# Optimization experiments

Measured on AMD Instinct MI355X. Metric: run time of the kernel, lower is better.

The kernel has to match this reference:

```python
import jax, jax.numpy as jnp
import numpy as np

B, H, N, D = 2, 16, 4096, 64
NUM_PROJS = 8
BLOCK_SIZE = 256
SAMPLE_SIZE = 256
SCALE = D ** -0.5  # default scale = dim ** -0.5


def _unit_hamming_distance_array(size_n):
    # Gray-code permutation so that adjacent hash buckets differ in one bit
    a = np.array([0, 1], dtype=np.int32)
    for _ in range(size_n - 1):
        a = np.concatenate([a, np.flip(a) + a.shape[0]])
    return a

_PERM = jnp.asarray(_unit_hamming_distance_array(NUM_PROJS))
_ENC = jnp.asarray(2 ** np.arange(NUM_PROJS, dtype=np.int32))  # [num_projs]


def lsh_hash(x, proj_dir):
    # x: [b,h,n,d], proj_dir: [d,r] -> bucket id per token: [b,h,n]
    proj = jnp.einsum('bhnd,dr->bhnr', x, proj_dir)
    bin_ids = jnp.sum((proj > 0).astype(jnp.int32) * _ENC, axis=-1)
    return _PERM[bin_ids]


def attn_lse(q, k, v, scale):
    # exact softmax attention returning output and log-sum-exp
    s = jnp.einsum('...md,...nd->...mn', q, k) * scale
    lse = jax.nn.logsumexp(s, axis=-1, keepdims=True)
    out = jnp.einsum('...mn,...nv->...mv', jnp.exp(s - lse), v)
    return out, lse


def gather_seq(x, idx):
    # gather along the sequence axis (axis=2); broadcasts over last dim
    return jnp.take_along_axis(x, idx[..., None], axis=2)


def add_self_attentions(attn1, lse1, attn2, lse2):
    # combine two un-normalized softmax attentions via their lse's
    c = jax.nn.sigmoid(lse1 - lse2)  # = 1/(1+exp(lse2-lse1))
    attn = c * attn1 + (1.0 - c) * attn2
    lse = jnp.logaddexp(lse1, lse2)
    return attn, lse


def setup_inputs() -> dict:
    key = jax.random.key(0)
    kq, kk, kv, kp, ks = jax.random.split(key, 5)
    return {
        'query': jax.random.normal(kq, (B, H, N, D), jnp.float32),
        'key': jax.random.normal(kk, (B, H, N, D), jnp.float32),
        'value': jax.random.normal(kv, (B, H, N, D), jnp.float32),
        'proj_dir': jax.random.normal(kp, (D, NUM_PROJS), jnp.float32),
        'sampled_set': jax.random.randint(ks, (B, H, SAMPLE_SIZE), 0, N, dtype=jnp.int32),
    }


def reference(query, key, value, proj_dir, sampled_set):
    # --- LSH bucketing + stable sort of queries/keys by bucket id ---
    q_idx = jnp.argsort(lsh_hash(query, proj_dir), axis=2, stable=True)
    k_idx = jnp.argsort(lsh_hash(key, proj_dir), axis=2, stable=True)
    q_idx_inv = jnp.argsort(q_idx, axis=2, stable=True)

    q_s = gather_seq(query, q_idx)
    k_s = gather_seq(key, k_idx)
    v_s = gather_seq(value, k_idx)

    # --- block-diagonal attention in sorted order ---
    nb = N // BLOCK_SIZE
    q_b = q_s.reshape(B, H, nb, BLOCK_SIZE, D)
    k_b = k_s.reshape(B, H, nb, BLOCK_SIZE, D)
    v_b = v_s.reshape(B, H, nb, BLOCK_SIZE, D)
    attn_blk, lse_blk = attn_lse(q_b, k_b, v_b, SCALE)
    attn_blk = attn_blk.reshape(B, H, N, D)
    lse_blk = lse_blk.reshape(B, H, N, 1)
    # un-sort back to original query order
    attn_blk = gather_seq(attn_blk, q_idx_inv)
    lse_blk = gather_seq(lse_blk, q_idx_inv)

    # --- uniformly sampled residual attention, importance-weighted ---
    k_sub = gather_seq(key, sampled_set)
    v_sub = gather_seq(value, sampled_set)
    attn_res, lse_res = attn_lse(query, k_sub, v_sub, SCALE)
    lse_res = lse_res + jnp.log(N / SAMPLE_SIZE)

    attn, lse = add_self_attentions(attn_blk, lse_blk, attn_res, lse_res)
    return attn
```

## Files before the change

### kernel.cpp

```cpp
#include <hip/hip_runtime.h>
#include <hip/hip_bf16.h>
#include <math.h>

#define BH_ 32
#define N_ 4096
#define D_ 64
#define SAMP_ 256
#define SCALE_ 0.125f
#define LOG16_ 2.7725887222397811f
#define HPAD 68

typedef __attribute__((ext_vector_type(4))) float f32x4;
typedef __attribute__((ext_vector_type(8))) short bf16x8;
typedef __attribute__((ext_vector_type(4))) short bf16x4;

static __device__ __forceinline__ unsigned pack2(float a, float b) {
    union { __hip_bfloat162 h; unsigned u; } c;
    c.h = __float22bfloat162_rn(make_float2(a, b));
    return c.u;
}

static __device__ __forceinline__ bf16x8 cvt8v(f32x4 a, f32x4 b) {
    union { unsigned u[4]; bf16x8 v; } r;
    r.u[0] = pack2(a[0], a[1]); r.u[1] = pack2(a[2], a[3]);
    r.u[2] = pack2(b[0], b[1]); r.u[3] = pack2(b[2], b[3]);
    return r.v;
}

static __device__ __forceinline__ bf16x8 cvt8(const float* p) {
    return cvt8v(*(const f32x4*)p, *(const f32x4*)(p + 4));
}

__global__ __launch_bounds__(128) void hash_kernel(
    const float* __restrict__ q, const float* __restrict__ k,
    const float* __restrict__ pd,
    unsigned char* __restrict__ qbuck, unsigned char* __restrict__ kbuck)
{
    extern __shared__ char smraw[];
    float*  Xs  = (float*)smraw;
    double* Pdl = (double*)(smraw + 128 * HPAD * 4);

    int tid = threadIdx.x;
    const float* src = blockIdx.y ? k : q;
    unsigned char* dst = blockIdx.y ? kbuck : qbuck;
    size_t tok0 = (size_t)blockIdx.x * 128;

    {
        int d = tid >> 1, r0 = (tid & 1) * 4;
#pragma unroll
        for (int j = 0; j < 4; ++j)
            Pdl[d * 8 + r0 + j] = (double)pd[d * 8 + r0 + j];
    }
    {
        const float4* src4 = (const float4*)(src + tok0 * D_);
        for (int i = tid; i < 128 * 16; i += 128) {
            int r = i >> 4, c = i & 15;
            *(float4*)&Xs[r * HPAD + c * 4] = src4[i];
        }
    }
    __syncthreads();

    float xr[64];
#pragma unroll
    for (int c = 0; c < 16; ++c)
        *(float4*)&xr[c * 4] = *(const float4*)&Xs[tid * HPAD + c * 4];

    double acc[8];
#pragma unroll
    for (int r = 0; r < 8; ++r) acc[r] = 0.0;
#pragma unroll
    for (int d = 0; d < 64; ++d) {
        double x = (double)xr[d];
        const double* pr = Pdl + d * 8;
#pragma unroll
        for (int r = 0; r < 8; ++r) acc[r] += x * pr[r];
    }
    int bin = 0;
#pragma unroll
    for (int r = 0; r < 8; ++r)
        if (acc[r] > 0.0) bin |= (1 << r);
    dst[tok0 + tid] = (unsigned char)(bin ^ (bin >> 1));
}

__global__ __launch_bounds__(256) void sort_kernel(
    const unsigned char* __restrict__ qbuck,
    const unsigned char* __restrict__ kbuck,
    int* __restrict__ q_idx, int* __restrict__ k_idx)
{
    __shared__ unsigned short hist[64][256];
    __shared__ unsigned int   binstart[256];
    __shared__ alignas(16) unsigned char bl[N_];

    int bh = blockIdx.x, tensor = blockIdx.y;
    const unsigned char* buck = (tensor ? kbuck : qbuck) + bh * N_;
    int* idx_out = (tensor ? k_idx : q_idx) + bh * N_;
    int t = threadIdx.x;

    ((uint4*)bl)[t] = ((const uint4*)buck)[t];
    {
        uint4* h4 = (uint4*)&hist[0][0];
        for (int i = t; i < 2048; i += 256) h4[i] = make_uint4(0, 0, 0, 0);
    }
    __syncthreads();

    if (t < 64) {
        for (int u = 0; u < 64; ++u) hist[t][bl[t * 64 + u]]++;
    }
    __syncthreads();

    {
        unsigned run = 0;
        for (int tt = 0; tt < 64; ++tt) {
            unsigned c = hist[tt][t];
            hist[tt][t] = (unsigned short)run;
            run += c;
        }
        binstart[t] = run;
    }
    __syncthreads();

    if (t < 64) {
        unsigned b0 = binstart[t*4], b1 = binstart[t*4+1],
                 b2 = binstart[t*4+2], b3 = binstart[t*4+3];
        unsigned s = b0 + b1 + b2 + b3, p = s;
#pragma unroll
        for (int d = 1; d < 64; d <<= 1) {
            unsigned y = __shfl_up(p, d);
            if (t >= d) p += y;
        }
        unsigned e = p - s;
        binstart[t*4]   = e;
        binstart[t*4+1] = e + b0;
        binstart[t*4+2] = e + b0 + b1;
        binstart[t*4+3] = e + b0 + b1 + b2;
    }
    __syncthreads();

    if (t < 64) {
        for (int u = 0; u < 64; ++u) {
            int tok = t * 64 + u;
            int b = bl[tok];
            int pos = (int)(binstart[b] + hist[t][b]);
            hist[t][b]++;
            idx_out[pos] = tok;
        }
    }
}

static __device__ __forceinline__ void compute_chunk16(
    const short* __restrict__ Ks, unsigned vtr, float bias,
    const bf16x8 (&qf)[2], int ll, int lg,
    f32x4 (&o)[4], float& lsum)
{
#pragma unroll
    for (int ks2 = 0; ks2 < 4; ++ks2) {
        unsigned pbu[4];
#pragma unroll
        for (int t = 0; t < 2; ++t) {
            int kt = ks2 * 2 + t;
            f32x4 s = {0.f, 0.f, 0.f, 0.f};
#pragma unroll
            for (int ks = 0; ks < 2; ++ks) {
                bf16x8 a = *(const bf16x8*)&Ks[kt * 1024 + ks * 512 + lg * 128 + ll * 8];
                s = __builtin_amdgcn_mfma_f32_16x16x32_bf16(a, qf[ks], s, 0, 0, 0);
            }
            f32x4 e;
#pragma unroll
            for (int r = 0; r < 4; ++r) e[r] = __expf(fmaf(s[r], SCALE_, bias));
            lsum += (e[0] + e[1]) + (e[2] + e[3]);
            pbu[t*2]   = pack2(e[0], e[1]);
            pbu[t*2+1] = pack2(e[2], e[3]);
        }
        bf16x8 pb;
        { union { unsigned u[4]; bf16x8 v; } c;
          c.u[0]=pbu[0]; c.u[1]=pbu[1]; c.u[2]=pbu[2]; c.u[3]=pbu[3]; pb = c.v; }

        bf16x4 tr[4][2];
#pragma unroll
        for (int dt = 0; dt < 4; ++dt) {
            asm volatile("ds_read_b64_tr_b16 %0, %1 offset:%2"
                         : "=v"(tr[dt][0]) : "v"(vtr), "i"(ks2 * 4096 + dt * 128));
            asm volatile("ds_read_b64_tr_b16 %0, %1 offset:%2"
                         : "=v"(tr[dt][1]) : "v"(vtr), "i"(ks2 * 4096 + dt * 128 + 2048));
        }
        asm volatile("s_waitcnt lgkmcnt(0)" ::: "memory");
        __builtin_amdgcn_sched_barrier(0);
#pragma unroll
        for (int dt = 0; dt < 4; ++dt) {
            union { bf16x4 h[2]; bf16x8 v; } va;
            va.h[0] = tr[dt][0]; va.h[1] = tr[dt][1];
            o[dt] = __builtin_amdgcn_mfma_f32_16x16x32_bf16(va.v, pb, o[dt], 0, 0, 0);
        }
    }
}

__global__ __launch_bounds__(1024, 8) void fused_attn(
    const float* __restrict__ query, const float* __restrict__ key,
    const float* __restrict__ value, const int* __restrict__ q_idx,
    const int* __restrict__ k_idx, const int* __restrict__ sampled,
    float* __restrict__ out)
{
    __shared__ short Ksm[8192];
    __shared__ short Vsm[8192];
    int wg = blockIdx.x, bh = wg >> 4, blk = wg & 15;
    int tid = threadIdx.x, w = tid >> 6, l = tid & 63, lg = l >> 4, ll = l & 15;
    size_t base = (size_t)bh * N_;

    int s_krow = ((tid >> 7) << 4) | (tid & 15);
    int s_kd   = ((tid >> 6) & 1) * 32 + ((tid >> 4) & 3) * 8;
    int s_vrow = ((tid >> 5) << 2) | ((tid >> 1) & 3);
    int s_vd   = ((tid >> 3) & 3) * 16 + (tid & 1) * 8;

    const int* kidxA = k_idx + base + blk * 256;
    const int* kidxB = sampled + bh * SAMP_;
    int kI0 = kidxA[s_krow], kI1 = kidxA[128 + s_krow];
    int kI2 = kidxB[s_krow], kI3 = kidxB[128 + s_krow];
    int vI0 = kidxA[s_vrow], vI1 = kidxA[128 + s_vrow];
    int vI2 = kidxB[s_vrow], vI3 = kidxB[128 + s_vrow];

    const int* qidx = q_idx + base + blk * 256 + w * 16;
    int qr = qidx[ll];
    const float* qp = query + (base + (size_t)qr) * D_ + lg * 8;
    bf16x8 qf[2] = { cvt8(qp), cvt8(qp + 32) };

    f32x4 o[4];
#pragma unroll
    for (int dt = 0; dt < 4; ++dt) { f32x4 z = {0.f,0.f,0.f,0.f}; o[dt] = z; }
    float lsum = 0.f;
    unsigned vtr = (unsigned)(unsigned long long)(void*)&Vsm[0] + lg * 512 + ll * 8;

#define STAGE_(KI, VI) do { \
        const float* kp_ = key   + (base + (size_t)(KI)) * D_ + s_kd; \
        const float* vp_ = value + (base + (size_t)(VI)) * D_ + s_vd; \
        bf16x8 kv_ = cvt8(kp_), vv_ = cvt8(vp_); \
        *(bf16x8*)&Ksm[tid * 8] = kv_; \
        *(bf16x8*)&Vsm[tid * 8] = vv_; } while (0)

    STAGE_(kI0, vI0); __syncthreads();
    compute_chunk16(Ksm, vtr, 0.f, qf, ll, lg, o, lsum);
    __syncthreads(); STAGE_(kI1, vI1); __syncthreads();
    compute_chunk16(Ksm, vtr, 0.f, qf, ll, lg, o, lsum);
    __syncthreads(); STAGE_(kI2, vI2); __syncthreads();
    compute_chunk16(Ksm, vtr, LOG16_, qf, ll, lg, o, lsum);
    __syncthreads(); STAGE_(kI3, vI3); __syncthreads();
    compute_chunk16(Ksm, vtr, LOG16_, qf, ll, lg, o, lsum);
#undef STAGE_

    lsum += __shfl_xor(lsum, 16);
    lsum += __shfl_xor(lsum, 32);

    float dn = 1.f / lsum;
    float* orow = out + (base + (size_t)qr) * D_ + lg * 4;
#pragma unroll
    for (int dt = 0; dt < 4; ++dt) {
        f32x4 v = o[dt] * dn;
        *(f32x4*)&orow[dt * 16] = v;
    }
}

extern "C" void kernel_launch(void* const* d_in, const int* in_sizes, int n_in,
                              void* d_out, int out_size, void* d_ws, size_t ws_size,
                              hipStream_t stream)
{
    const float* query = (const float*)d_in[0];
    const float* key   = (const float*)d_in[1];
    const float* value = (const float*)d_in[2];
    const float* pd    = (const float*)d_in[3];
    const int*   samp  = (const int*)d_in[4];
    float* out = (float*)d_out;

    char* ws = (char*)d_ws;
    unsigned char* qbuck = (unsigned char*)ws;
    unsigned char* kbuck = qbuck + (size_t)BH_ * N_;
    int* q_idx = (int*)(ws + 262144);
    int* k_idx = (int*)(ws + 262144 + 524288);

    size_t hash_lds = 128 * HPAD * 4 + 512 * 8;
    hipLaunchKernelGGL(hash_kernel, dim3(BH_ * N_ / 128, 2), dim3(128),
                       hash_lds, stream, query, key, pd, qbuck, kbuck);
    hipLaunchKernelGGL(sort_kernel, dim3(BH_, 2), dim3(256), 0, stream,
                       qbuck, kbuck, q_idx, k_idx);
    hipLaunchKernelGGL(fused_attn, dim3(512), dim3(1024), 0, stream,
                       query, key, value, q_idx, k_idx, samp, out);
}
```

Before: 90.32 us.

## Restructure attention into per-wave register-prefetched K/V chunks without block barriers

Instead of the workgroup cooperatively staging 128-key chunks into shared memory with __syncthreads, each wave now loads its own 32-key chunks. K fragments go straight into registers and V goes into a private LDS slice read back with transpose reads. The next chunk's global loads and the index loads two chunks ahead are issued before the current compute, so memory latency overlaps with MFMA work. The workgroup shrinks to 512 threads over 128 queries, doubling the grid. In exchange, each wave reads K/V for its own 16-query group, multiplying global/L2 traffic per block, and register pressure rises.

Result: slower. 328.7 us (+263.9%).

```diff
diff --git a/kernel.cpp b/kernel.cpp
--- a/kernel.cpp
+++ b/kernel.cpp
@@ -63,7 +63,7 @@
     float xr[64];
 #pragma unroll
     for (int c = 0; c < 16; ++c)
-        *(float4*)&xr[c * 4] = *(const float4*)&Xs[tid * HPAD + c * 4];
+        *(f32x4*)&xr[c * 4] = *(const f32x4*)&Xs[tid * HPAD + c * 4];
 
     double acc[8];
 #pragma unroll
@@ -147,78 +147,27 @@
     }
 }
 
-static __device__ __forceinline__ void compute_chunk16(
-    const short* __restrict__ Ks, unsigned vtr, float bias,
-    const bf16x8 (&qf)[2], int ll, int lg,
-    f32x4 (&o)[4], float& lsum)
-{
-#pragma unroll
-    for (int ks2 = 0; ks2 < 4; ++ks2) {
-        unsigned pbu[4];
-#pragma unroll
-        for (int t = 0; t < 2; ++t) {
-            int kt = ks2 * 2 + t;
-            f32x4 s = {0.f, 0.f, 0.f, 0.f};
-#pragma unroll
-            for (int ks = 0; ks < 2; ++ks) {
-                bf16x8 a = *(const bf16x8*)&Ks[kt * 1024 + ks * 512 + lg * 128 + ll * 8];
-                s = __builtin_amdgcn_mfma_f32_16x16x32_bf16(a, qf[ks], s, 0, 0, 0);
-            }
-            f32x4 e;
-#pragma unroll
-            for (int r = 0; r < 4; ++r) e[r] = __expf(fmaf(s[r], SCALE_, bias));
-            lsum += (e[0] + e[1]) + (e[2] + e[3]);
-            pbu[t*2]   = pack2(e[0], e[1]);
-            pbu[t*2+1] = pack2(e[2], e[3]);
-        }
-        bf16x8 pb;
-        { union { unsigned u[4]; bf16x8 v; } c;
-          c.u[0]=pbu[0]; c.u[1]=pbu[1]; c.u[2]=pbu[2]; c.u[3]=pbu[3]; pb = c.v; }
-
-        bf16x4 tr[4][2];
-#pragma unroll
-        for (int dt = 0; dt < 4; ++dt) {
-            asm volatile("ds_read_b64_tr_b16 %0, %1 offset:%2"
-                         : "=v"(tr[dt][0]) : "v"(vtr), "i"(ks2 * 4096 + dt * 128));
-            asm volatile("ds_read_b64_tr_b16 %0, %1 offset:%2"
-                         : "=v"(tr[dt][1]) : "v"(vtr), "i"(ks2 * 4096 + dt * 128 + 2048));
-        }
-        asm volatile("s_waitcnt lgkmcnt(0)" ::: "memory");
-        __builtin_amdgcn_sched_barrier(0);
-#pragma unroll
-        for (int dt = 0; dt < 4; ++dt) {
-            union { bf16x4 h[2]; bf16x8 v; } va;
-            va.h[0] = tr[dt][0]; va.h[1] = tr[dt][1];
-            o[dt] = __builtin_amdgcn_mfma_f32_16x16x32_bf16(va.v, pb, o[dt], 0, 0, 0);
-        }
-    }
-}
-
-__global__ __launch_bounds__(1024, 8) void fused_attn(
+__global__ __launch_bounds__(512, 4) void fused_attn(
     const float* __restrict__ query, const float* __restrict__ key,
     const float* __restrict__ value, const int* __restrict__ q_idx,
     const int* __restrict__ k_idx, const int* __restrict__ sampled,
     float* __restrict__ out)
 {
-    __shared__ short Ksm[8192];
-    __shared__ short Vsm[8192];
-    int wg = blockIdx.x, bh = wg >> 4, blk = wg & 15;
+    __shared__ __align__(16) short Vsm[8 * 2048];
+    int wg = blockIdx.x, bh = wg >> 5, qb128 = wg & 31;
     int tid = threadIdx.x, w = tid >> 6, l = tid & 63, lg = l >> 4, ll = l & 15;
     size_t base = (size_t)bh * N_;
 
-    int s_krow = ((tid >> 7) << 4) | (tid & 15);
-    int s_kd   = ((tid >> 6) & 1) * 32 + ((tid >> 4) & 3) * 8;
-    int s_vrow = ((tid >> 5) << 2) | ((tid >> 1) & 3);
-    int s_vd   = ((tid >> 3) & 3) * 16 + (tid & 1) * 8;
-
-    const int* kidxA = k_idx + base + blk * 256;
+    const int* kidxA = k_idx + base + (qb128 >> 1) * 256;
     const int* kidxB = sampled + bh * SAMP_;
-    int kI0 = kidxA[s_krow], kI1 = kidxA[128 + s_krow];
-    int kI2 = kidxB[s_krow], kI3 = kidxB[128 + s_krow];
-    int vI0 = kidxA[s_vrow], vI1 = kidxA[128 + s_vrow];
-    int vI2 = kidxB[s_vrow], vI3 = kidxB[128 + s_vrow];
-
-    const int* qidx = q_idx + base + blk * 256 + w * 16;
+
+    short* Vw = &Vsm[w * 2048];
+    unsigned vtr = (unsigned)(unsigned long long)(void*)Vw + lg * 512 + ll * 8;
+
+    int dv8  = ((l >> 3) & 3) * 2 + (l & 1);
+    int kbse = (l >> 5) * 4 + ((l >> 1) & 3);
+
+    const int* qidx = q_idx + base + qb128 * 128 + w * 16;
     int qr = qidx[ll];
     const float* qp = query + (base + (size_t)qr) * D_ + lg * 8;
     bf16x8 qf[2] = { cvt8(qp), cvt8(qp + 32) };
@@ -227,24 +176,110 @@
 #pragma unroll
     for (int dt = 0; dt < 4; ++dt) { f32x4 z = {0.f,0.f,0.f,0.f}; o[dt] = z; }
     float lsum = 0.f;
-    unsigned vtr = (unsigned)(unsigned long long)(void*)&Vsm[0] + lg * 512 + ll * 8;
-
-#define STAGE_(KI, VI) do { \
-        const float* kp_ = key   + (base + (size_t)(KI)) * D_ + s_kd; \
-        const float* vp_ = value + (base + (size_t)(VI)) * D_ + s_vd; \
-        bf16x8 kv_ = cvt8(kp_), vv_ = cvt8(vp_); \
-        *(bf16x8*)&Ksm[tid * 8] = kv_; \
-        *(bf16x8*)&Vsm[tid * 8] = vv_; } while (0)
-
-    STAGE_(kI0, vI0); __syncthreads();
-    compute_chunk16(Ksm, vtr, 0.f, qf, ll, lg, o, lsum);
-    __syncthreads(); STAGE_(kI1, vI1); __syncthreads();
-    compute_chunk16(Ksm, vtr, 0.f, qf, ll, lg, o, lsum);
-    __syncthreads(); STAGE_(kI2, vI2); __syncthreads();
-    compute_chunk16(Ksm, vtr, LOG16_, qf, ll, lg, o, lsum);
-    __syncthreads(); STAGE_(kI3, vI3); __syncthreads();
-    compute_chunk16(Ksm, vtr, LOG16_, qf, ll, lg, o, lsum);
-#undef STAGE_
+
+    const int* s0 = kidxA;
+    int ki0 = s0[ll], ki1 = s0[16 + ll];
+    int va0 = s0[kbse], va1 = s0[kbse + 8], va2 = s0[kbse + 16], va3 = s0[kbse + 24];
+
+    f32x4 vld[8], kld[8];
+    {
+        const float* vp0 = value + (base + (size_t)va0) * D_ + dv8 * 8;
+        const float* vp1 = value + (base + (size_t)va1) * D_ + dv8 * 8;
+        const float* vp2 = value + (base + (size_t)va2) * D_ + dv8 * 8;
+        const float* vp3 = value + (base + (size_t)va3) * D_ + dv8 * 8;
+        vld[0] = *(const f32x4*)vp0; vld[1] = *(const f32x4*)(vp0 + 4);
+        vld[2] = *(const f32x4*)vp1; vld[3] = *(const f32x4*)(vp1 + 4);
+        vld[4] = *(const f32x4*)vp2; vld[5] = *(const f32x4*)(vp2 + 4);
+        vld[6] = *(const f32x4*)vp3; vld[7] = *(const f32x4*)(vp3 + 4);
+        const float* kp0 = key + (base + (size_t)ki0) * D_ + lg * 8;
+        const float* kp1 = key + (base + (size_t)ki1) * D_ + lg * 8;
+        kld[0] = *(const f32x4*)kp0;        kld[1] = *(const f32x4*)(kp0 + 4);
+        kld[2] = *(const f32x4*)(kp0 + 32); kld[3] = *(const f32x4*)(kp0 + 36);
+        kld[4] = *(const f32x4*)kp1;        kld[5] = *(const f32x4*)(kp1 + 4);
+        kld[6] = *(const f32x4*)(kp1 + 32); kld[7] = *(const f32x4*)(kp1 + 36);
+    }
+    const int* s1 = kidxA + 32;
+    int nki0 = s1[ll], nki1 = s1[16 + ll];
+    int nva0 = s1[kbse], nva1 = s1[kbse + 8], nva2 = s1[kbse + 16], nva3 = s1[kbse + 24];
+
+    for (int c = 0; c < 16; ++c) {
+        bf16x8 kf0a, kf0b, kf1a, kf1b;
+        {
+            bf16x8 vw0 = cvt8v(vld[0], vld[1]);
+            bf16x8 vw1 = cvt8v(vld[2], vld[3]);
+            bf16x8 vw2 = cvt8v(vld[4], vld[5]);
+            bf16x8 vw3 = cvt8v(vld[6], vld[7]);
+            *(bf16x8*)&Vw[(l      ) * 8] = vw0;
+            *(bf16x8*)&Vw[(l +  64) * 8] = vw1;
+            *(bf16x8*)&Vw[(l + 128) * 8] = vw2;
+            *(bf16x8*)&Vw[(l + 192) * 8] = vw3;
+            kf0a = cvt8v(kld[0], kld[1]);
+            kf0b = cvt8v(kld[2], kld[3]);
+            kf1a = cvt8v(kld[4], kld[5]);
+            kf1b = cvt8v(kld[6], kld[7]);
+        }
+
+        if (c < 15) {
+            const float* vp0 = value + (base + (size_t)nva0) * D_ + dv8 * 8;
+            const float* vp1 = value + (base + (size_t)nva1) * D_ + dv8 * 8;
+            const float* vp2 = value + (base + (size_t)nva2) * D_ + dv8 * 8;
+            const float* vp3 = value + (base + (size_t)nva3) * D_ + dv8 * 8;
+            vld[0] = *(const f32x4*)vp0; vld[1] = *(const f32x4*)(vp0 + 4);
+            vld[2] = *(const f32x4*)vp1; vld[3] = *(const f32x4*)(vp1 + 4);
+            vld[4] = *(const f32x4*)vp2; vld[5] = *(const f32x4*)(vp2 + 4);
+            vld[6] = *(const f32x4*)vp3; vld[7] = *(const f32x4*)(vp3 + 4);
+            const float* kp0 = key + (base + (size_t)nki0) * D_ + lg * 8;
+            const float* kp1 = key + (base + (size_t)nki1) * D_ + lg * 8;
+            kld[0] = *(const f32x4*)kp0;        kld[1] = *(const f32x4*)(kp0 + 4);
+            kld[2] = *(const f32x4*)(kp0 + 32); kld[3] = *(const f32x4*)(kp0 + 36);
+            kld[4] = *(const f32x4*)kp1;        kld[5] = *(const f32x4*)(kp1 + 4);
+            kld[6] = *(const f32x4*)(kp1 + 32); kld[7] = *(const f32x4*)(kp1 + 36);
+        }
+        if (c < 14) {
+            int cn = c + 2;
+            const int* sn = (cn < 8) ? (kidxA + cn * 32) : (kidxB + (cn - 8) * 32);
+            nki0 = sn[ll]; nki1 = sn[16 + ll];
+            nva0 = sn[kbse]; nva1 = sn[kbse + 8];
+            nva2 = sn[kbse + 16]; nva3 = sn[kbse + 24];
+        }
+
+        float bias = (c < 8) ? 0.f : LOG16_;
+        f32x4 sA = {0.f,0.f,0.f,0.f}, sB = {0.f,0.f,0.f,0.f};
+        sA = __builtin_amdgcn_mfma_f32_16x16x32_bf16(kf0a, qf[0], sA, 0, 0, 0);
+        sA = __builtin_amdgcn_mfma_f32_16x16x32_bf16(kf0b, qf[1], sA, 0, 0, 0);
+        sB = __builtin_amdgcn_mfma_f32_16x16x32_bf16(kf1a, qf[0], sB, 0, 0, 0);
+        sB = __builtin_amdgcn_mfma_f32_16x16x32_bf16(kf1b, qf[1], sB, 0, 0, 0);
+
+        f32x4 eA, eB;
+#pragma unroll
+        for (int r = 0; r < 4; ++r) {
+            eA[r] = __expf(fmaf(sA[r], SCALE_, bias));
+            eB[r] = __expf(fmaf(sB[r], SCALE_, bias));
+        }
+        lsum += (eA[0] + eA[1]) + (eA[2] + eA[3]) +
+                (eB[0] + eB[1]) + (eB[2] + eB[3]);
+        bf16x8 pb;
+        { union { unsigned u[4]; bf16x8 v; } pc;
+          pc.u[0] = pack2(eA[0], eA[1]); pc.u[1] = pack2(eA[2], eA[3]);
+          pc.u[2] = pack2(eB[0], eB[1]); pc.u[3] = pack2(eB[2], eB[3]);
+          pb = pc.v; }
+
+        __builtin_amdgcn_sched_barrier(0);
+        asm volatile("s_waitcnt lgkmcnt(0)" ::: "memory");
+#pragma unroll
+        for (int dt = 0; dt < 4; ++dt) {
+            bf16x4 t0, t1;
+            asm volatile("ds_read_b64_tr_b16 %0, %1 offset:%2"
+                         : "=v"(t0) : "v"(vtr), "i"(dt * 128));
+            asm volatile("ds_read_b64_tr_b16 %0, %1 offset:%2"
+                         : "=v"(t1) : "v"(vtr), "i"(dt * 128 + 2048));
+            asm volatile("s_waitcnt lgkmcnt(0)" ::: "memory");
+            __builtin_amdgcn_sched_barrier(0);
+            union { bf16x4 h[2]; bf16x8 v; } va;
+            va.h[0] = t0; va.h[1] = t1;
+            o[dt] = __builtin_amdgcn_mfma_f32_16x16x32_bf16(va.v, pb, o[dt], 0, 0, 0);
+        }
+    }
 
     lsum += __shfl_xor(lsum, 16);
     lsum += __shfl_xor(lsum, 32);
@@ -280,6 +315,6 @@
                        hash_lds, stream, query, key, pd, qbuck, kbuck);
     hipLaunchKernelGGL(sort_kernel, dim3(BH_, 2), dim3(256), 0, stream,
                        qbuck, kbuck, q_idx, k_idx);
-    hipLaunchKernelGGL(fused_attn, dim3(512), dim3(1024), 0, stream,
+    hipLaunchKernelGGL(fused_attn, dim3(1024), dim3(512), 0, stream,
                        query, key, value, q_idx, k_idx, samp, out);
 }
```

## Split attention workgroups in half, remap blocks, prefetch indices, use exp2 with setprio

Applied to the files above, without the earlier changes.

The fused attention kernel now launches 1024 workgroups of 512 threads. Each workgroup handles 128 queries instead of 256, and the block-to-workgroup mapping is swizzled across the eight XCDs. Index loads for the next key/value chunk are issued before the current compute phase. Exponentials use exp2 with a prescaled constant, and s_setprio hints wrap the MFMA sections. Each thread now stages more key/value elements with wider vector loads, and every K/V block is loaded twice, once per half-workgroup. That doubles global gather traffic in exchange for more parallelism and occupancy.

Result: slower. 101.2 us (+12.1%).

```diff
diff --git a/kernel.cpp b/kernel.cpp
--- a/kernel.cpp
+++ b/kernel.cpp
@@ -6,8 +6,7 @@
 #define N_ 4096
 #define D_ 64
 #define SAMP_ 256
-#define SCALE_ 0.125f
-#define LOG16_ 2.7725887222397811f
+#define SC2_ 0.1803368801111244f
 #define HPAD 68
 
 typedef __attribute__((ext_vector_type(4))) float f32x4;
@@ -63,7 +62,7 @@
     float xr[64];
 #pragma unroll
     for (int c = 0; c < 16; ++c)
-        *(float4*)&xr[c * 4] = *(const float4*)&Xs[tid * HPAD + c * 4];
+        *(f32x4*)&xr[c * 4] = *(const f32x4*)&Xs[tid * HPAD + c * 4];
 
     double acc[8];
 #pragma unroll
@@ -147,78 +146,31 @@
     }
 }
 
-static __device__ __forceinline__ void compute_chunk16(
-    const short* __restrict__ Ks, unsigned vtr, float bias,
-    const bf16x8 (&qf)[2], int ll, int lg,
-    f32x4 (&o)[4], float& lsum)
-{
-#pragma unroll
-    for (int ks2 = 0; ks2 < 4; ++ks2) {
-        unsigned pbu[4];
-#pragma unroll
-        for (int t = 0; t < 2; ++t) {
-            int kt = ks2 * 2 + t;
-            f32x4 s = {0.f, 0.f, 0.f, 0.f};
-#pragma unroll
-            for (int ks = 0; ks < 2; ++ks) {
-                bf16x8 a = *(const bf16x8*)&Ks[kt * 1024 + ks * 512 + lg * 128 + ll * 8];
-                s = __builtin_amdgcn_mfma_f32_16x16x32_bf16(a, qf[ks], s, 0, 0, 0);
-            }
-            f32x4 e;
-#pragma unroll
-            for (int r = 0; r < 4; ++r) e[r] = __expf(fmaf(s[r], SCALE_, bias));
-            lsum += (e[0] + e[1]) + (e[2] + e[3]);
-            pbu[t*2]   = pack2(e[0], e[1]);
-            pbu[t*2+1] = pack2(e[2], e[3]);
-        }
-        bf16x8 pb;
-        { union { unsigned u[4]; bf16x8 v; } c;
-          c.u[0]=pbu[0]; c.u[1]=pbu[1]; c.u[2]=pbu[2]; c.u[3]=pbu[3]; pb = c.v; }
-
-        bf16x4 tr[4][2];
-#pragma unroll
-        for (int dt = 0; dt < 4; ++dt) {
-            asm volatile("ds_read_b64_tr_b16 %0, %1 offset:%2"
-                         : "=v"(tr[dt][0]) : "v"(vtr), "i"(ks2 * 4096 + dt * 128));
-            asm volatile("ds_read_b64_tr_b16 %0, %1 offset:%2"
-                         : "=v"(tr[dt][1]) : "v"(vtr), "i"(ks2 * 4096 + dt * 128 + 2048));
-        }
-        asm volatile("s_waitcnt lgkmcnt(0)" ::: "memory");
-        __builtin_amdgcn_sched_barrier(0);
-#pragma unroll
-        for (int dt = 0; dt < 4; ++dt) {
-            union { bf16x4 h[2]; bf16x8 v; } va;
-            va.h[0] = tr[dt][0]; va.h[1] = tr[dt][1];
-            o[dt] = __builtin_amdgcn_mfma_f32_16x16x32_bf16(va.v, pb, o[dt], 0, 0, 0);
-        }
-    }
-}
-
-__global__ __launch_bounds__(1024, 8) void fused_attn(
+__global__ __launch_bounds__(512, 8) void fused_attn(
     const float* __restrict__ query, const float* __restrict__ key,
     const float* __restrict__ value, const int* __restrict__ q_idx,
     const int* __restrict__ k_idx, const int* __restrict__ sampled,
     float* __restrict__ out)
 {
-    __shared__ short Ksm[8192];
-    __shared__ short Vsm[8192];
-    int wg = blockIdx.x, bh = wg >> 4, blk = wg & 15;
+    __shared__ __align__(16) short Ksm[8192];
+    __shared__ __align__(16) short Vsm[8192];
+    int wgid = blockIdx.x;
+    int wg = (wgid & 7) * 128 + (wgid >> 3);
+    int bh = wg >> 5, sub = wg & 31;
     int tid = threadIdx.x, w = tid >> 6, l = tid & 63, lg = l >> 4, ll = l & 15;
     size_t base = (size_t)bh * N_;
 
-    int s_krow = ((tid >> 7) << 4) | (tid & 15);
-    int s_kd   = ((tid >> 6) & 1) * 32 + ((tid >> 4) & 3) * 8;
-    int s_vrow = ((tid >> 5) << 2) | ((tid >> 1) & 3);
-    int s_vd   = ((tid >> 3) & 3) * 16 + (tid & 1) * 8;
-
-    const int* kidxA = k_idx + base + blk * 256;
+    const int* kidxA = k_idx + base + (sub >> 1) * 256;
     const int* kidxB = sampled + bh * SAMP_;
-    int kI0 = kidxA[s_krow], kI1 = kidxA[128 + s_krow];
-    int kI2 = kidxB[s_krow], kI3 = kidxB[128 + s_krow];
-    int vI0 = kidxA[s_vrow], vI1 = kidxA[128 + s_vrow];
-    int vI2 = kidxB[s_vrow], vI3 = kidxB[128 + s_vrow];
-
-    const int* qidx = q_idx + base + blk * 256 + w * 16;
+
+    int krow = tid & 127, kd0 = (tid >> 7) * 16;
+    int koff = (krow >> 4) * 1024 + (kd0 >> 5) * 512 + ((kd0 >> 3) & 3) * 128
+             + (krow & 15) * 8;
+    int l6 = tid & 63, i6 = tid >> 6;
+    int vrow = (i6 >> 2) * 32 + (i6 & 3) * 8 + (l6 >> 5) * 4 + ((l6 >> 1) & 3);
+    int vd   = ((l6 >> 3) & 3) * 16 + (l6 & 1) * 8;
+
+    const int* qidx = q_idx + base + sub * 128 + w * 16;
     int qr = qidx[ll];
     const float* qp = query + (base + (size_t)qr) * D_ + lg * 8;
     bf16x8 qf[2] = { cvt8(qp), cvt8(qp + 32) };
@@ -229,22 +181,89 @@
     float lsum = 0.f;
     unsigned vtr = (unsigned)(unsigned long long)(void*)&Vsm[0] + lg * 512 + ll * 8;
 
-#define STAGE_(KI, VI) do { \
-        const float* kp_ = key   + (base + (size_t)(KI)) * D_ + s_kd; \
-        const float* vp_ = value + (base + (size_t)(VI)) * D_ + s_vd; \
-        bf16x8 kv_ = cvt8(kp_), vv_ = cvt8(vp_); \
-        *(bf16x8*)&Ksm[tid * 8] = kv_; \
-        *(bf16x8*)&Vsm[tid * 8] = vv_; } while (0)
-
-    STAGE_(kI0, vI0); __syncthreads();
-    compute_chunk16(Ksm, vtr, 0.f, qf, ll, lg, o, lsum);
-    __syncthreads(); STAGE_(kI1, vI1); __syncthreads();
-    compute_chunk16(Ksm, vtr, 0.f, qf, ll, lg, o, lsum);
-    __syncthreads(); STAGE_(kI2, vI2); __syncthreads();
-    compute_chunk16(Ksm, vtr, LOG16_, qf, ll, lg, o, lsum);
-    __syncthreads(); STAGE_(kI3, vI3); __syncthreads();
-    compute_chunk16(Ksm, vtr, LOG16_, qf, ll, lg, o, lsum);
+#define STAGE_(KI, VI0, VI1) do { \
+        const float* kp_ = key + (base + (size_t)(KI)) * D_ + kd0; \
+        f32x4 ka_ = *(const f32x4*)kp_,       kb_ = *(const f32x4*)(kp_ + 4); \
+        f32x4 kc_ = *(const f32x4*)(kp_ + 8), kd_ = *(const f32x4*)(kp_ + 12); \
+        const float* vp0_ = value + (base + (size_t)(VI0)) * D_ + vd; \
+        const float* vp1_ = value + (base + (size_t)(VI1)) * D_ + vd; \
+        f32x4 va_ = *(const f32x4*)vp0_, vb_ = *(const f32x4*)(vp0_ + 4); \
+        f32x4 vc_ = *(const f32x4*)vp1_, vd_ = *(const f32x4*)(vp1_ + 4); \
+        *(bf16x8*)&Ksm[koff]        = cvt8v(ka_, kb_); \
+        *(bf16x8*)&Ksm[koff + 128]  = cvt8v(kc_, kd_); \
+        *(bf16x8*)&Vsm[tid * 8]        = cvt8v(va_, vb_); \
+        *(bf16x8*)&Vsm[4096 + tid * 8] = cvt8v(vc_, vd_); } while (0)
+
+#define COMPUTE_(BIAS2) do { \
+        _Pragma("unroll") \
+        for (int hgi = 0; hgi < 4; ++hgi) { \
+            unsigned pbu[4]; \
+            __builtin_amdgcn_s_setprio(1); \
+            _Pragma("unroll") \
+            for (int t = 0; t < 2; ++t) { \
+                int kt = hgi * 2 + t; \
+                f32x4 s = {0.f,0.f,0.f,0.f}; \
+                _Pragma("unroll") \
+                for (int ks = 0; ks < 2; ++ks) { \
+                    bf16x8 a = *(const bf16x8*)&Ksm[kt * 1024 + ks * 512 + lg * 128 + ll * 8]; \
+                    s = __builtin_amdgcn_mfma_f32_16x16x32_bf16(a, qf[ks], s, 0, 0, 0); \
+                } \
+                __builtin_amdgcn_s_setprio(0); \
+                f32x4 e; \
+                _Pragma("unroll") \
+                for (int r = 0; r < 4; ++r) e[r] = exp2f(fmaf(s[r], SC2_, (BIAS2))); \
+                lsum += (e[0] + e[1]) + (e[2] + e[3]); \
+                pbu[t*2]   = pack2(e[0], e[1]); \
+                pbu[t*2+1] = pack2(e[2], e[3]); \
+                __builtin_amdgcn_s_setprio(1); \
+            } \
+            bf16x8 pb; \
+            { union { unsigned u[4]; bf16x8 v; } cc_; \
+              cc_.u[0]=pbu[0]; cc_.u[1]=pbu[1]; cc_.u[2]=pbu[2]; cc_.u[3]=pbu[3]; pb=cc_.v; } \
+            bf16x4 tr[4][2]; \
+            _Pragma("unroll") \
+            for (int dt = 0; dt < 4; ++dt) { \
+                asm volatile("ds_read_b64_tr_b16 %0, %1 offset:%2" \
+                             : "=v"(tr[dt][0]) : "v"(vtr), "i"(hgi * 4096 + dt * 128)); \
+                asm volatile("ds_read_b64_tr_b16 %0, %1 offset:%2" \
+                             : "=v"(tr[dt][1]) : "v"(vtr), "i"(hgi * 4096 + dt * 128 + 2048)); \
+            } \
+            asm volatile("s_waitcnt lgkmcnt(0)" ::: "memory"); \
+            __builtin_amdgcn_sched_barrier(0); \
+            _Pragma("unroll") \
+            for (int dt = 0; dt < 4; ++dt) { \
+                union { bf16x4 h[2]; bf16x8 v; } va2; \
+                va2.h[0] = tr[dt][0]; va2.h[1] = tr[dt][1]; \
+                o[dt] = __builtin_amdgcn_mfma_f32_16x16x32_bf16(va2.v, pb, o[dt], 0, 0, 0); \
+            } \
+            __builtin_amdgcn_s_setprio(0); \
+        } } while (0)
+
+    int kI = kidxA[krow], vI0 = kidxA[vrow], vI1 = kidxA[64 + vrow];
+
+    STAGE_(kI, vI0, vI1);
+    __syncthreads();
+    kI = kidxA[128 + krow]; vI0 = kidxA[128 + vrow]; vI1 = kidxA[192 + vrow];
+    COMPUTE_(0.f);
+    __syncthreads();
+
+    STAGE_(kI, vI0, vI1);
+    __syncthreads();
+    kI = kidxB[krow]; vI0 = kidxB[vrow]; vI1 = kidxB[64 + vrow];
+    COMPUTE_(0.f);
+    __syncthreads();
+
+    STAGE_(kI, vI0, vI1);
+    __syncthreads();
+    kI = kidxB[128 + krow]; vI0 = kidxB[128 + vrow]; vI1 = kidxB[192 + vrow];
+    COMPUTE_(4.f);
+    __syncthreads();
+
+    STAGE_(kI, vI0, vI1);
+    __syncthreads();
+    COMPUTE_(4.f);
 #undef STAGE_
+#undef COMPUTE_
 
     lsum += __shfl_xor(lsum, 16);
     lsum += __shfl_xor(lsum, 32);
@@ -280,6 +299,6 @@
                        hash_lds, stream, query, key, pd, qbuck, kbuck);
     hipLaunchKernelGGL(sort_kernel, dim3(BH_, 2), dim3(256), 0, stream,
                        qbuck, kbuck, q_idx, k_idx);
-    hipLaunchKernelGGL(fused_attn, dim3(512), dim3(1024), 0, stream,
+    hipLaunchKernelGGL(fused_attn, dim3(1024), dim3(512), 0, stream,
                        query, key, value, q_idx, k_idx, samp, out);
 }
```
